# Performance work log

Hardware: AMD Instinct MI355X
Metric: run time of the kernel (lower is better)

The kernel has to match this reference:

```python
import math
import jax, jax.numpy as jnp
import numpy as np

LN_EPS = 1e-5
SIG_DOMAIN = 5.0


def _layer_norm(x, gamma, beta):
    mu = jnp.mean(x, axis=-1, keepdims=True)
    var = jnp.var(x, axis=-1, keepdims=True)
    return (x - mu) / jnp.sqrt(var + LN_EPS) * gamma + beta


def setup_inputs() -> dict:
    key = jax.random.key(0)
    k0, k1, k2, k3 = jax.random.split(key, 4)
    B, H, S, D = 4, 16, 1024, 256   # batch, c_heads, seq, input_dim
    A, O = 128, 256                 # attention_dim, output_dim
    x = jax.random.normal(k0, (B, H, S, D), dtype=jnp.float32)
    # torch.rand -> uniform [0,1)
    W_query = jax.random.uniform(k1, (H, A, D), dtype=jnp.float32)
    W_key = jax.random.uniform(k2, (H, A, D), dtype=jnp.float32)
    W_value = jax.random.uniform(k3, (H, O, D), dtype=jnp.float32)
    gamma = jnp.ones((D,), dtype=jnp.float32)
    beta = jnp.zeros((D,), dtype=jnp.float32)
    return {"x": x, "W_query": W_query, "W_key": W_key, "W_value": W_value,
            "gamma": gamma, "beta": beta}


def reference(x, W_query, W_key, W_value, gamma, beta):
    scale = math.sqrt(x.shape[-1])  # sqrt(input_dim)
    xn = _layer_norm(x, gamma, beta)                       # [B,H,S,D]
    q = jnp.einsum('bhsd,had->bhsa', xn, W_query)          # [B,H,S,A]
    k = jnp.einsum('bhsd,had->bhsa', xn, W_key)            # [B,H,S,A]
    v = jnp.einsum('bhsd,hod->bhso', xn, W_value)          # [B,H,S,O]
    scores = jnp.einsum('bhsa,bhta->bhst', q, k) / scale   # [B,H,S,S]
    # overtaking-sigmoid-tuned normalization
    s_max = jnp.max(scores, axis=-1, keepdims=True)
    s_min = jnp.min(scores, axis=-1, keepdims=True)
    s_norm = (scores - s_min) / (s_max - s_min)
    softmax_sel = 1.0 - jax.nn.sigmoid(
        (1.0 - jnp.max(s_norm, axis=-1, keepdims=True)) * 2.0 * SIG_DOMAIN + SIG_DOMAIN)
    sigmoid_sel = 1.0 - softmax_sel
    weights = (softmax_sel * jax.nn.softmax(s_norm, axis=-1)
               + sigmoid_sel * jax.nn.sigmoid(s_norm * 2.0 * SIG_DOMAIN - SIG_DOMAIN))
    return jnp.einsum('bhst,bhto->bhso', weights, v)       # [B,H,S,O]
```

## Files before the change

### kernel.cpp

```cpp
#include <hip/hip_runtime.h>

typedef __attribute__((ext_vector_type(8))) short bf16x8;
typedef __attribute__((ext_vector_type(8))) _Float16 h16x8;
typedef __attribute__((ext_vector_type(2))) _Float16 h16x2;
typedef __attribute__((ext_vector_type(2))) __fp16 fp16x2;
typedef __attribute__((ext_vector_type(4))) float f32x4;
typedef __attribute__((ext_vector_type(4))) unsigned short us4;
typedef unsigned short u16;

#define MFMA16  __builtin_amdgcn_mfma_f32_16x16x32_bf16
#define MFMA16H __builtin_amdgcn_mfma_f32_16x16x32_f16

__device__ __forceinline__ u16 f2bf(float f) {
  union { float f; unsigned u; } v; v.f = f;
  unsigned r = v.u + 0x7FFFu + ((v.u >> 16) & 1u);
  return (u16)(r >> 16);
}

__device__ __forceinline__ float ex2(float x) {
#if __has_builtin(__builtin_amdgcn_exp2f)
  return __builtin_amdgcn_exp2f(x);
#else
  return exp2f(x);
#endif
}

__global__ __launch_bounds__(256) void ln_kernel(const float* __restrict__ x,
    const float* __restrict__ gamma, const float* __restrict__ beta,
    u16* __restrict__ xn)
{
  int row = blockIdx.x * 4 + (threadIdx.x >> 6);
  int lane = threadIdx.x & 63;
  const float* xr = x + (size_t)row * 256;
  f32x4 v = *(const f32x4*)(xr + lane * 4);
  float s  = v[0] + v[1] + v[2] + v[3];
  float s2 = v[0]*v[0] + v[1]*v[1] + v[2]*v[2] + v[3]*v[3];
  #pragma unroll
  for (int off = 1; off < 64; off <<= 1) {
    s  += __shfl_xor(s, off);
    s2 += __shfl_xor(s2, off);
  }
  float mu   = s * (1.0f / 256.0f);
  float var  = s2 * (1.0f / 256.0f) - mu * mu;
  float rstd = rsqrtf(var + 1e-5f);
  f32x4 g  = *(const f32x4*)(gamma + lane * 4);
  f32x4 bb = *(const f32x4*)(beta  + lane * 4);
  us4 o;
  #pragma unroll
  for (int j = 0; j < 4; j++) o[j] = f2bf((v[j] - mu) * rstd * g[j] + bb[j]);
  *(us4*)(xn + (size_t)row * 256 + lane * 4) = o;
}

__global__ __launch_bounds__(256) void cvt_kernel(const float* __restrict__ in,
    u16* __restrict__ out, int n4)
{
  int i = blockIdx.x * 256 + threadIdx.x;
  if (i >= n4) return;
  f32x4 v = *(const f32x4*)(in + (size_t)i * 4);
  us4 o;
  #pragma unroll
  for (int j = 0; j < 4; j++) o[j] = f2bf(v[j]);
  *(us4*)(out + (size_t)i * 4) = o;
}

__global__ __launch_bounds__(256) void cvt_qk(const float* __restrict__ in,
    u16* __restrict__ out, int half)
{
  int i = blockIdx.x * 256 + threadIdx.x;
  int e4 = i * 4;
  int h = e4 >> 15;
  int rem = e4 & 32767;
  f32x4 v = *(const f32x4*)(in + e4);
  us4 o;
  #pragma unroll
  for (int j = 0; j < 4; j++) o[j] = f2bf(v[j]);
  *(us4*)(out + (size_t)h * 65536 + half * 32768 + rem) = o;
}

__global__ __launch_bounds__(256) void gemm128(const u16* __restrict__ Ag,
    const u16* __restrict__ Bg, u16* __restrict__ Cg,
    int M, int N, int aHead, int bHead, int outHalf)
{
  constexpr int K = 256;
  __shared__ u16 As[128][128];
  __shared__ u16 Bs[128][128];
  int bh = blockIdx.z;
  int m0 = blockIdx.x * 128, n0 = blockIdx.y * 128;
  const u16* Ab = Ag + (size_t)(aHead ? (bh & 15) : bh) * M * K + (size_t)m0 * K;
  const u16* Bb = Bg + (size_t)(bHead ? (bh & 15) : bh) * N * K + (size_t)n0 * K;
  int tid = threadIdx.x, lane = tid & 63, w = tid >> 6;
  int wm = w >> 1, wn = w & 1;
  int lr = lane & 15, g = lane >> 4;

  f32x4 acc[4][4] = {};
  for (int kc = 0; kc < 2; kc++) {
    if (kc) __syncthreads();
    #pragma unroll
    for (int i = 0; i < 8; i++) {
      int c = tid + 256 * i;
      int r = c >> 4, ch = c & 15;
      int sw = (ch ^ (r & 7)) * 8;
      *(bf16x8*)&As[r][sw] = *(const bf16x8*)(Ab + (size_t)r * K + kc * 128 + ch * 8);
      *(bf16x8*)&Bs[r][sw] = *(const bf16x8*)(Bb + (size_t)r * K + kc * 128 + ch * 8);
    }
    __syncthreads();
    #pragma unroll
    for (int ks = 0; ks < 4; ks++) {
      bf16x8 af[4], bfr[4];
      #pragma unroll
      for (int mf = 0; mf < 4; mf++) {
        int r = wm * 64 + mf * 16 + lr;
        af[mf] = *(const bf16x8*)&As[r][((ks * 4 + g) ^ (r & 7)) * 8];
      }
      #pragma unroll
      for (int nf = 0; nf < 4; nf++) {
        int r = wn * 64 + nf * 16 + lr;
        bfr[nf] = *(const bf16x8*)&Bs[r][((ks * 4 + g) ^ (r & 7)) * 8];
      }
      #pragma unroll
      for (int mf = 0; mf < 4; mf++)
        #pragma unroll
        for (int nf = 0; nf < 4; nf++)
          acc[mf][nf] = MFMA16(af[mf], bfr[nf], acc[mf][nf], 0, 0, 0);
    }
  }
  u16* Cb = Cg + (size_t)bh * M * N;
  #pragma unroll
  for (int mf = 0; mf < 4; mf++)
    #pragma unroll
    for (int nf = 0; nf < 4; nf++)
      #pragma unroll
      for (int i = 0; i < 4; i++) {
        int row = m0 + wm * 64 + mf * 16 + g * 4 + i;
        int col = n0 + wn * 64 + nf * 16 + lr;
        u16 ev;
        if (outHalf) { _Float16 hv = (_Float16)acc[mf][nf][i]; ev = *(u16*)&hv; }
        else ev = f2bf(acc[mf][nf][i]);
        Cb[(size_t)row * N + col] = ev;
      }
}

__global__ __launch_bounds__(256) void score_kernel(
    const u16* __restrict__ QKg, _Float16* __restrict__ Sg, float2* __restrict__ rp, int bh0)
{
  constexpr int S = 1024, LD = 256;
  __shared__ u16 Qs[128][128];
  __shared__ u16 Ks[128][128];
  int bid = blockIdx.x;
  int hl = ((bid >> 6) << 3) | (bid & 7);
  int rb = (bid >> 3) & 7;
  int bh = bh0 + hl;
  int m0 = rb * 128;
  int tid = threadIdx.x, lane = tid & 63, w = tid >> 6;
  int lr = lane & 15, g = lane >> 4;
  const u16* Qb = QKg + ((size_t)bh * S + m0) * LD;
  const u16* Kb = QKg + (size_t)bh * S * LD + 128;

  #pragma unroll
  for (int i = 0; i < 8; i++) {
    int c = tid + 256 * i;
    int r = c >> 4, ch = c & 15;
    *(bf16x8*)&Qs[r][(ch ^ (r & 7)) * 8] = *(const bf16x8*)(Qb + (size_t)r * LD + ch * 8);
    *(bf16x8*)&Ks[r][(ch ^ (r & 7)) * 8] = *(const bf16x8*)(Kb + (size_t)r * LD + ch * 8);
  }
  __syncthreads();

  bf16x8 aq[2][4];
  #pragma unroll
  for (int mf = 0; mf < 2; mf++)
    #pragma unroll
    for (int ks = 0; ks < 4; ks++) {
      int r = w * 32 + mf * 16 + lr;
      aq[mf][ks] = *(const bf16x8*)&Qs[r][((ks * 4 + g) ^ (r & 7)) * 8];
    }

  float rmin[2][4], rmax[2][4];
  #pragma unroll
  for (int mf = 0; mf < 2; mf++)
    #pragma unroll
    for (int i = 0; i < 4; i++) { rmin[mf][i] = 3.0e38f; rmax[mf][i] = -3.0e38f; }

  _Float16* Sb = Sg + (size_t)hl * S * S;
  for (int nc = 0; nc < 8; nc++) {
    bf16x8 kreg[8];
    if (nc < 7) {
      #pragma unroll
      for (int i = 0; i < 8; i++) {
        int c = tid + 256 * i;
        int r = c >> 4, ch = c & 15;
        kreg[i] = *(const bf16x8*)(Kb + (size_t)(128 * (nc + 1) + r) * LD + ch * 8);
      }
    }
    f32x4 acc[2][8] = {};
    #pragma unroll
    for (int ks = 0; ks < 4; ks++) {
      bf16x8 bk[8];
      #pragma unroll
      for (int nf = 0; nf < 8; nf++) {
        int r = nf * 16 + lr;
        bk[nf] = *(const bf16x8*)&Ks[r][((ks * 4 + g) ^ (r & 7)) * 8];
      }
      #pragma unroll
      for (int mf = 0; mf < 2; mf++)
        #pragma unroll
        for (int nf = 0; nf < 8; nf++)
          acc[mf][nf] = MFMA16(aq[mf][ks], bk[nf], acc[mf][nf], 0, 0, 0);
    }
    #pragma unroll
    for (int mf = 0; mf < 2; mf++)
      #pragma unroll
      for (int nf = 0; nf < 8; nf++)
        #pragma unroll
        for (int i = 0; i < 4; i++) {
          int row = m0 + w * 32 + mf * 16 + g * 4 + i;
          int col = nc * 128 + nf * 16 + lr;
          Sb[(size_t)row * S + col] = (_Float16)acc[mf][nf][i];
          rmin[mf][i] = fminf(rmin[mf][i], acc[mf][nf][i]);
          rmax[mf][i] = fmaxf(rmax[mf][i], acc[mf][nf][i]);
        }
    __syncthreads();
    if (nc < 7) {
      #pragma unroll
      for (int i = 0; i < 8; i++) {
        int c = tid + 256 * i;
        int r = c >> 4, ch = c & 15;
        *(bf16x8*)&Ks[r][(ch ^ (r & 7)) * 8] = kreg[i];
      }
    }
    __syncthreads();
  }
  #pragma unroll
  for (int off = 1; off < 16; off <<= 1)
    #pragma unroll
    for (int mf = 0; mf < 2; mf++)
      #pragma unroll
      for (int i = 0; i < 4; i++) {
        rmin[mf][i] = fminf(rmin[mf][i], __shfl_xor(rmin[mf][i], off));
        rmax[mf][i] = fmaxf(rmax[mf][i], __shfl_xor(rmax[mf][i], off));
      }
  if (lr == 0) {
    #pragma unroll
    for (int mf = 0; mf < 2; mf++)
      #pragma unroll
      for (int i = 0; i < 4; i++) {
        int row = m0 + w * 32 + mf * 16 + g * 4 + i;
        float inv = 1.0f / (rmax[mf][i] - rmin[mf][i]);
        rp[(size_t)bh * S + row] = make_float2(10.0f * inv, fmaf(-10.0f * rmin[mf][i], inv, -5.0f));
      }
  }
}

__global__ __launch_bounds__(256) void pv_kernel(
    const _Float16* __restrict__ Sg, const float2* __restrict__ rpG,
    const u16* __restrict__ VTg, float* __restrict__ Out, int bh0)
{
  constexpr int S = 1024, OD = 256;
  __shared__ u16 Bs[2][256 * 34];
  int bid = blockIdx.x;
  int hl = ((bid >> 6) << 3) | (bid & 7);
  int rb = (bid >> 3) & 7;
  int bh = bh0 + hl;
  int m0 = rb * 128;
  int tid = threadIdx.x, lane = tid & 63, w = tid >> 6;
  int lr = lane & 15, g = lane >> 4;
  const _Float16* Sb = Sg + (size_t)hl * S * S;
  const u16* Vb = VTg + (size_t)bh * OD * S;

  float am[2], bm[2];
  const _Float16* Srow[2];
  #pragma unroll
  for (int mf = 0; mf < 2; mf++) {
    int row = m0 + w * 32 + mf * 16 + lr;
    float2 p = rpG[(size_t)bh * S + row];
    am[mf] = -p.x * 1.44269504f;
    bm[mf] = -p.y * 1.44269504f;
    Srow[mf] = Sb + (size_t)row * S + g * 8;
  }

  f32x4 acc[2][16] = {};

  bf16x8 pre[4];
  h16x8 svc[2], svn[2];
  #pragma unroll
  for (int i = 0; i < 4; i++) pre[i] = *(const bf16x8*)(Vb + (size_t)tid * S + i * 8);
  #pragma unroll
  for (int i = 0; i < 4; i++) *(bf16x8*)&Bs[0][tid * 34 + i * 8] = pre[i];
  svc[0] = *(const h16x8*)(Srow[0]);
  svc[1] = *(const h16x8*)(Srow[1]);
  __syncthreads();

  for (int kt = 0; kt < 32; kt++) {
    int cur = kt & 1;
    if (kt < 31) {
      #pragma unroll
      for (int i = 0; i < 4; i++)
        pre[i] = *(const bf16x8*)(Vb + (size_t)tid * S + (kt + 1) * 32 + i * 8);
      svn[0] = *(const h16x8*)(Srow[0] + (kt + 1) * 32);
      svn[1] = *(const h16x8*)(Srow[1] + (kt + 1) * 32);
    }
    h16x8 pa[2];
    #pragma unroll
    for (int mf = 0; mf < 2; mf++) {
      h16x2* pw = (h16x2*)&pa[mf];
      #pragma unroll
      for (int q = 0; q < 4; q++) {
        float e0 = ex2(fmaf((float)svc[mf][2*q],     am[mf], bm[mf]));
        float e1 = ex2(fmaf((float)svc[mf][2*q + 1], am[mf], bm[mf]));
        fp16x2 pk = __builtin_amdgcn_cvt_pkrtz(__builtin_amdgcn_rcpf(1.0f + e0),
                                               __builtin_amdgcn_rcpf(1.0f + e1));
        pw[q] = __builtin_bit_cast(h16x2, pk);
      }
    }
    __builtin_amdgcn_s_setprio(1);
    #pragma unroll
    for (int nf = 0; nf < 16; nf++) {
      h16x8 bv = *(const h16x8*)&Bs[cur][(nf * 16 + lr) * 34 + g * 8];
      acc[0][nf] = MFMA16H(pa[0], bv, acc[0][nf], 0, 0, 0);
      acc[1][nf] = MFMA16H(pa[1], bv, acc[1][nf], 0, 0, 0);
    }
    __builtin_amdgcn_s_setprio(0);
    if (kt < 31) {
      #pragma unroll
      for (int i = 0; i < 4; i++) *(bf16x8*)&Bs[cur ^ 1][tid * 34 + i * 8] = pre[i];
      svc[0] = svn[0]; svc[1] = svn[1];
    }
    __syncthreads();
  }

  const float c2 = 0.9933071490757153f;
  float* Ob = Out + ((size_t)bh * S + m0 + w * 32) * OD;
  #pragma unroll
  for (int mf = 0; mf < 2; mf++)
    #pragma unroll
    for (int nf = 0; nf < 16; nf++)
      #pragma unroll
      for (int i = 0; i < 4; i++) {
        int row = mf * 16 + g * 4 + i;
        int col = nf * 16 + lr;
        Ob[(size_t)row * OD + col] = c2 * acc[mf][nf][i];
      }
}

extern "C" void kernel_launch(void* const* d_in, const int* in_sizes, int n_in,
                              void* d_out, int out_size, void* d_ws, size_t ws_size,
                              hipStream_t stream) {
  const float* x     = (const float*)d_in[0];
  const float* Wq    = (const float*)d_in[1];
  const float* Wk    = (const float*)d_in[2];
  const float* Wv    = (const float*)d_in[3];
  const float* gamma = (const float*)d_in[4];
  const float* beta  = (const float*)d_in[5];
  float* out = (float*)d_out;

  constexpr int B = 4, H = 16, S = 1024, D = 256, A = 128, O = 256;
  constexpr int BH = B * H;

  char* p = (char*)d_ws;
  size_t off = 0;
  auto take = [&](size_t n) { off = (off + 255) & ~(size_t)255; char* q = p + off; off += n; return q; };

  u16*    xn   = (u16*)take((size_t)BH * S * D * 2);
  u16*    qkb  = (u16*)take((size_t)BH * S * 256 * 2);
  u16*    vtb  = (u16*)take((size_t)BH * O * S * 2);
  u16*    wqkb = (u16*)take((size_t)H * 256 * D * 2);
  u16*    wvb  = (u16*)take((size_t)H * O * D * 2);
  float2* rp   = (float2*)take((size_t)BH * S * 8);

  int grp = 1;
  for (; grp < 8; grp <<= 1) {
    size_t need = ((off + 255) & ~(size_t)255) + (size_t)(BH / grp) * S * S * 2;
    if (need <= ws_size) break;
  }
  int hp = BH / grp;
  _Float16* sG = (_Float16*)take((size_t)hp * S * S * 2);

  ln_kernel<<<BH * S / 4, 256, 0, stream>>>(x, gamma, beta, xn);

  cvt_qk<<<(H * A * D / 4) / 256, 256, 0, stream>>>(Wq, wqkb, 0);
  cvt_qk<<<(H * A * D / 4) / 256, 256, 0, stream>>>(Wk, wqkb, 1);
  cvt_kernel<<<(H * O * D / 4 + 255) / 256, 256, 0, stream>>>(Wv, wvb, H * O * D / 4);

  gemm128<<<dim3(S / 128, 256 / 128, BH), 256, 0, stream>>>(xn, wqkb, qkb, S, 256, 0, 1, 0);
  gemm128<<<dim3(O / 128, S / 128, BH), 256, 0, stream>>>(wvb, xn, vtb, O, S, 1, 0, 1);

  for (int gi = 0; gi < grp; gi++) {
    int bh0 = gi * hp;
    score_kernel<<<hp * 8, 256, 0, stream>>>(qkb, sG, rp, bh0);
    pv_kernel<<<hp * 8, 256, 0, stream>>>(sG, rp, vtb, out, bh0);
  }
}
```

Before: 175.2 us.

## Restructure PV kernel: stage sigmoid probabilities in LDS, stream V from registers

Reworks the P·V kernel so the sigmoid weights are computed cooperatively once per 64-row tile and stored to a double-buffered LDS array. V fragments are now loaded straight from global memory into registers as the MFMA A operand, which swaps the operand roles. Tiles shrink from 128 to 64 rows, doubling the block count, and a launch-bounds occupancy hint is added. Output stores become 16-byte vectorized writes. The aim is to cut LDS traffic for V and raise occupancy and store efficiency. The cost is that each V tile is read twice as often across blocks, and the per-lane V loads are strided.

```diff
diff --git a/kernel.cpp b/kernel.cpp
--- a/kernel.cpp
+++ b/kernel.cpp
@@ -23,6 +23,20 @@
 #else
   return exp2f(x);
 #endif
+}
+
+__device__ __forceinline__ h16x8 sigmoid8(h16x8 sv, float am, float bm) {
+  h16x8 pa;
+  h16x2* pw = (h16x2*)&pa;
+  #pragma unroll
+  for (int q = 0; q < 4; q++) {
+    float e0 = ex2(fmaf((float)sv[2*q],     am, bm));
+    float e1 = ex2(fmaf((float)sv[2*q + 1], am, bm));
+    fp16x2 pk = __builtin_amdgcn_cvt_pkrtz(__builtin_amdgcn_rcpf(1.0f + e0),
+                                           __builtin_amdgcn_rcpf(1.0f + e1));
+    pw[q] = __builtin_bit_cast(h16x2, pk);
+  }
+  return pa;
 }
 
 __global__ __launch_bounds__(256) void ln_kernel(const float* __restrict__ x,
@@ -250,95 +264,83 @@
   }
 }
 
-__global__ __launch_bounds__(256) void pv_kernel(
+__global__ __launch_bounds__(256, 4) void pv_kernel(
     const _Float16* __restrict__ Sg, const float2* __restrict__ rpG,
-    const u16* __restrict__ VTg, float* __restrict__ Out, int bh0)
-{
-  constexpr int S = 1024, OD = 256;
-  __shared__ u16 Bs[2][256 * 34];
+    const _Float16* __restrict__ VTg, float* __restrict__ Out, int bh0)
+{
+  constexpr int S = 1024, OD = 256, PSTR = 40;
+  __shared__ _Float16 P_lds[2][64 * PSTR];
   int bid = blockIdx.x;
-  int hl = ((bid >> 6) << 3) | (bid & 7);
-  int rb = (bid >> 3) & 7;
+  int hl = ((bid >> 7) << 3) | (bid & 7);
+  int rb = (bid >> 3) & 15;
   int bh = bh0 + hl;
-  int m0 = rb * 128;
+  int m0 = rb * 64;
   int tid = threadIdx.x, lane = tid & 63, w = tid >> 6;
   int lr = lane & 15, g = lane >> 4;
   const _Float16* Sb = Sg + (size_t)hl * S * S;
-  const u16* Vb = VTg + (size_t)bh * OD * S;
-
-  float am[2], bm[2];
-  const _Float16* Srow[2];
-  #pragma unroll
-  for (int mf = 0; mf < 2; mf++) {
-    int row = m0 + w * 32 + mf * 16 + lr;
-    float2 p = rpG[(size_t)bh * S + row];
-    am[mf] = -p.x * 1.44269504f;
-    bm[mf] = -p.y * 1.44269504f;
-    Srow[mf] = Sb + (size_t)row * S + g * 8;
-  }
-
-  f32x4 acc[2][16] = {};
-
-  bf16x8 pre[4];
-  h16x8 svc[2], svn[2];
-  #pragma unroll
-  for (int i = 0; i < 4; i++) pre[i] = *(const bf16x8*)(Vb + (size_t)tid * S + i * 8);
-  #pragma unroll
-  for (int i = 0; i < 4; i++) *(bf16x8*)&Bs[0][tid * 34 + i * 8] = pre[i];
-  svc[0] = *(const h16x8*)(Srow[0]);
-  svc[1] = *(const h16x8*)(Srow[1]);
+  const _Float16* Vb = VTg + (size_t)bh * OD * S;
+
+  int r0 = tid >> 2, c = tid & 3;
+  float2 pp = rpG[(size_t)bh * S + m0 + r0];
+  float am = -pp.x * 1.44269504f, bm = -pp.y * 1.44269504f;
+  const _Float16* Srow = Sb + (size_t)(m0 + r0) * S + c * 8;
+  _Float16* Pw0 = &P_lds[0][r0 * PSTR + c * 8];
+  _Float16* Pw1 = &P_lds[1][r0 * PSTR + c * 8];
+
+  const _Float16* Vrow[4];
+  #pragma unroll
+  for (int of = 0; of < 4; of++)
+    Vrow[of] = Vb + (size_t)(w * 64 + of * 16 + lr) * S + g * 8;
+
+  f32x4 acc[4][4] = {};
+
+  h16x8 sv0 = *(const h16x8*)(Srow);
+  h16x8 sv1 = *(const h16x8*)(Srow + 32);
+  h16x8 va[4], vb[4];
+  #pragma unroll
+  for (int of = 0; of < 4; of++) va[of] = *(const h16x8*)(Vrow[of]);
+  *(h16x8*)Pw0 = sigmoid8(sv0, am, bm);
   __syncthreads();
 
   for (int kt = 0; kt < 32; kt++) {
     int cur = kt & 1;
     if (kt < 31) {
       #pragma unroll
-      for (int i = 0; i < 4; i++)
-        pre[i] = *(const bf16x8*)(Vb + (size_t)tid * S + (kt + 1) * 32 + i * 8);
-      svn[0] = *(const h16x8*)(Srow[0] + (kt + 1) * 32);
-      svn[1] = *(const h16x8*)(Srow[1] + (kt + 1) * 32);
-    }
-    h16x8 pa[2];
-    #pragma unroll
-    for (int mf = 0; mf < 2; mf++) {
-      h16x2* pw = (h16x2*)&pa[mf];
-      #pragma unroll
-      for (int q = 0; q < 4; q++) {
-        float e0 = ex2(fmaf((float)svc[mf][2*q],     am[mf], bm[mf]));
-        float e1 = ex2(fmaf((float)svc[mf][2*q + 1], am[mf], bm[mf]));
-        fp16x2 pk = __builtin_amdgcn_cvt_pkrtz(__builtin_amdgcn_rcpf(1.0f + e0),
-                                               __builtin_amdgcn_rcpf(1.0f + e1));
-        pw[q] = __builtin_bit_cast(h16x2, pk);
-      }
-    }
+      for (int of = 0; of < 4; of++)
+        vb[of] = *(const h16x8*)(Vrow[of] + (kt + 1) * 32);
+    }
+    h16x8 svn;
+    if (kt < 30) svn = *(const h16x8*)(Srow + (kt + 2) * 32);
+    if (kt < 31)
+      *(h16x8*)(cur ? Pw0 : Pw1) = sigmoid8(sv1, am, bm);
     __builtin_amdgcn_s_setprio(1);
     #pragma unroll
-    for (int nf = 0; nf < 16; nf++) {
-      h16x8 bv = *(const h16x8*)&Bs[cur][(nf * 16 + lr) * 34 + g * 8];
-      acc[0][nf] = MFMA16H(pa[0], bv, acc[0][nf], 0, 0, 0);
-      acc[1][nf] = MFMA16H(pa[1], bv, acc[1][nf], 0, 0, 0);
+    for (int rf = 0; rf < 4; rf++) {
+      h16x8 pb = *(const h16x8*)&P_lds[cur][(rf * 16 + lr) * PSTR + g * 8];
+      #pragma unroll
+      for (int of = 0; of < 4; of++)
+        acc[of][rf] = MFMA16H(va[of], pb, acc[of][rf], 0, 0, 0);
     }
     __builtin_amdgcn_s_setprio(0);
-    if (kt < 31) {
-      #pragma unroll
-      for (int i = 0; i < 4; i++) *(bf16x8*)&Bs[cur ^ 1][tid * 34 + i * 8] = pre[i];
-      svc[0] = svn[0]; svc[1] = svn[1];
-    }
+    #pragma unroll
+    for (int of = 0; of < 4; of++) va[of] = vb[of];
+    sv0 = sv1; sv1 = svn;
     __syncthreads();
   }
 
   const float c2 = 0.9933071490757153f;
-  float* Ob = Out + ((size_t)bh * S + m0 + w * 32) * OD;
-  #pragma unroll
-  for (int mf = 0; mf < 2; mf++)
-    #pragma unroll
-    for (int nf = 0; nf < 16; nf++)
-      #pragma unroll
-      for (int i = 0; i < 4; i++) {
-        int row = mf * 16 + g * 4 + i;
-        int col = nf * 16 + lr;
-        Ob[(size_t)row * OD + col] = c2 * acc[mf][nf][i];
-      }
+  float* Ob = Out + (size_t)bh * S * OD;
+  #pragma unroll
+  for (int of = 0; of < 4; of++)
+    #pragma unroll
+    for (int rf = 0; rf < 4; rf++) {
+      f32x4 v = acc[of][rf];
+      #pragma unroll
+      for (int i = 0; i < 4; i++) v[i] *= c2;
+      int row = m0 + rf * 16 + lr;
+      int col = w * 64 + of * 16 + g * 4;
+      *(f32x4*)(Ob + (size_t)row * OD + col) = v;
+    }
 }
 
 extern "C" void kernel_launch(void* const* d_in, const int* in_sizes, int n_in,
@@ -386,6 +388,7 @@
   for (int gi = 0; gi < grp; gi++) {
     int bh0 = gi * hp;
     score_kernel<<<hp * 8, 256, 0, stream>>>(qkb, sG, rp, bh0);
-    pv_kernel<<<hp * 8, 256, 0, stream>>>(sG, rp, vtb, out, bh0);
-  }
-}
+    pv_kernel<<<hp * 16, 256, 0, stream>>>((const _Float16*)sG, rp,
+                                           (const _Float16*)vtb, out, bh0);
+  }
+}
```

Result: slower. 190.9 us (+9.0%).
